# Performance work log

Hardware: AMD Instinct MI355X
Metric: run time of the kernel (lower is better)

## Reference

```python
import jax, jax.numpy as jnp
import numpy as np

N = 50000      # nodes
E = 800000     # edges (before self-loops)
IN_F = 64
HID = 96
OUT_F = 16
L = 16         # num GCN2Conv layers
ALPHA = 0.1
THETA = 0.5


def setup_inputs() -> dict:
    key = jax.random.key(0)
    ks = jax.random.split(key, 6)
    x = jax.random.normal(ks[0], (N, IN_F), jnp.float32)
    edge_index = jax.random.randint(ks[1], (2, E), 0, N, jnp.int64)
    lin0_w = jax.random.normal(ks[2], (HID, IN_F), jnp.float32) * 0.05
    lin0_b = jnp.zeros((HID,), jnp.float32)
    lin1_w = jax.random.normal(ks[3], (OUT_F, HID), jnp.float32) * 0.05
    lin1_b = jnp.zeros((OUT_F,), jnp.float32)
    conv_w = jax.random.normal(ks[4], (L, HID, HID), jnp.float32) * 0.05
    return {"x": x, "edge_index": edge_index, "lin0_w": lin0_w, "lin0_b": lin0_b,
            "lin1_w": lin1_w, "lin1_b": lin1_b, "conv_w": conv_w}


def _gcn_norm(edge_index, n):
    # add self-loops, symmetric normalization D^-1/2 A D^-1/2 (edge weights = 1)
    loops = jnp.arange(n, dtype=edge_index.dtype)
    row = jnp.concatenate([edge_index[0], loops])
    col = jnp.concatenate([edge_index[1], loops])
    ones = jnp.ones(row.shape[0], jnp.float32)
    deg = jax.ops.segment_sum(ones, col, num_segments=n)
    dis = jnp.where(deg > 0, jax.lax.rsqrt(deg), 0.0)
    val = dis[row] * dis[col]
    return row, col, val


def reference(x, edge_index, lin0_w, lin0_b, lin1_w, lin1_b, conv_w):
    n = x.shape[0]
    row, col, val = _gcn_norm(edge_index, n)
    h = jax.nn.relu(x @ lin0_w.T + lin0_b)            # [N, HID]
    x0 = h
    betas = jnp.log(THETA / jnp.arange(1.0, L + 1.0) + 1.0).astype(jnp.float32)

    def layer(h, wb):
        w, beta = wb
        # SpMM: out[i] = sum_{(i,j) in E} val * h[j]
        m = jax.ops.segment_sum(val[:, None] * h[col], row, num_segments=n)
        s = (1.0 - ALPHA) * m + ALPHA * x0            # initial-residual combine
        out = (1.0 - beta) * s + beta * (s @ w)       # identity mapping (shared weights)
        return jax.nn.relu(out), None

    h, _ = jax.lax.scan(layer, h, (conv_w, betas))
    return h @ lin1_w.T + lin1_b
```

## Files before the change

kernel.cpp:

```cpp
#include <hip/hip_runtime.h>

#define NTHREADS 256
#define HID 96
#define INF 64
#define OUTF 16
#define NLAYERS 16
#define NHW 25088
#define CB 128

typedef __attribute__((ext_vector_type(8))) unsigned short ushort8_t;
typedef __attribute__((ext_vector_type(8))) short short8_t;
typedef __attribute__((ext_vector_type(4))) float f32x4_t;

static __device__ __forceinline__ float bf2f(unsigned short u) {
  return __uint_as_float(((unsigned)u) << 16);
}
static __device__ __forceinline__ unsigned short f2bf(float x) {
  unsigned u = __float_as_uint(x);
  return (unsigned short)((u + 0x7FFF + ((u >> 16) & 1)) >> 16);
}
static __device__ __forceinline__ unsigned pack2bf(float a, float b) {
  return (unsigned)f2bf(a) | ((unsigned)f2bf(b) << 16);
}

__global__ __launch_bounds__(NTHREADS) void k_hist(
    const int* __restrict__ idx, int e, unsigned* __restrict__ part, int nw) {
  __shared__ unsigned hh[NHW];
  int tid = threadIdx.x;
  for (int i = tid; i < NHW; i += NTHREADS) hh[i] = 0;
  __syncthreads();
  int per = (e + CB - 1) / CB;
  int s = blockIdx.x * per;
  int en = min(e, s + per);
  for (int i = s + tid; i < en; i += NTHREADS) {
    int v = idx[i];
    atomicAdd(&hh[v >> 1], (v & 1) ? 0x10000u : 1u);
  }
  __syncthreads();
  unsigned* dst = part + (size_t)blockIdx.x * NHW;
  for (int i = tid; i < nw; i += NTHREADS) dst[i] = hh[i];
}

__global__ void k_hmerge(unsigned* __restrict__ partR,
                         const unsigned* __restrict__ partC,
                         int* __restrict__ cnt, int* __restrict__ deg,
                         int n, int nw) {
  int w = blockIdx.x * NTHREADS + threadIdx.x;
  if (w >= nw) return;
  unsigned rl = 0, rh = 0, cl = 0, ch = 0;
#pragma unroll 4
  for (int b = 0; b < CB; ++b) {
    size_t o = (size_t)b * NHW + w;
    unsigned pr = partR[o];
    partR[o] = rl | (rh << 16);
    rl += pr & 0xFFFFu; rh += pr >> 16;
    unsigned pc = partC[o];
    cl += pc & 0xFFFFu; ch += pc >> 16;
  }
  int i0 = 2 * w, i1 = 2 * w + 1;
  if (i0 < n) { cnt[i0] = 1 + (int)rl; deg[i0] = 1 + (int)cl; }
  if (i1 < n) { cnt[i1] = 1 + (int)rh; deg[i1] = 1 + (int)ch; }
}

__global__ void k_dis(const int* __restrict__ deg, float* __restrict__ dis,
                      float* __restrict__ selfval, int n) {
  int i = blockIdx.x * NTHREADS + threadIdx.x;
  if (i < n) {
    float d = (float)deg[i];
    dis[i] = rsqrtf(d);
    selfval[i] = 1.0f / d;
  }
}

__global__ void k_scan1(const int* __restrict__ cnt, int* __restrict__ rp,
                        int* __restrict__ bsum, int n) {
  __shared__ int sh[NTHREADS];
  int t = threadIdx.x;
  int i = blockIdx.x * NTHREADS + t;
  int v = (i < n) ? cnt[i] : 0;
  sh[t] = v;
  __syncthreads();
  for (int ofs = 1; ofs < NTHREADS; ofs <<= 1) {
    int u = (t >= ofs) ? sh[t - ofs] : 0;
    __syncthreads();
    sh[t] += u;
    __syncthreads();
  }
  if (i < n) rp[i] = sh[t] - v;
  if (t == NTHREADS - 1) bsum[blockIdx.x] = sh[t];
}

__global__ void k_scan2(int* __restrict__ bsum, int nb) {
  __shared__ int sh[NTHREADS];
  int t = threadIdx.x;
  int v = (t < nb) ? bsum[t] : 0;
  sh[t] = v;
  __syncthreads();
  for (int ofs = 1; ofs < NTHREADS; ofs <<= 1) {
    int u = (t >= ofs) ? sh[t - ofs] : 0;
    __syncthreads();
    sh[t] += u;
    __syncthreads();
  }
  if (t < nb) bsum[t] = sh[t] - v;
}

__global__ void k_scan3(int* __restrict__ rp, const int* __restrict__ bsum,
                        int n, int etot) {
  int i = blockIdx.x * NTHREADS + threadIdx.x;
  if (i < n) rp[i] += bsum[blockIdx.x];
  if (i == 0) rp[n] = etot;
}

__global__ void k_self(const int* __restrict__ rp, const float* __restrict__ sv,
                       int2* __restrict__ ev, int n) {
  int i = blockIdx.x * NTHREADS + threadIdx.x;
  if (i < n) {
    int2 v;
    v.x = i;
    v.y = __float_as_int(sv[i]);
    ev[rp[i]] = v;
  }
}

__global__ __launch_bounds__(NTHREADS) void k_scatter2(
    const int* __restrict__ row, const int* __restrict__ col,
    const int* __restrict__ rp, const unsigned* __restrict__ prefR,
    const float* __restrict__ dis, int2* __restrict__ ev, int e) {
  __shared__ unsigned lcur[NHW];
  int tid = threadIdx.x;
  for (int i = tid; i < NHW; i += NTHREADS) lcur[i] = 0;
  __syncthreads();
  int per = (e + CB - 1) / CB;
  int s = blockIdx.x * per;
  int en = min(e, s + per);
  const unsigned* pref = prefR + (size_t)blockIdx.x * NHW;
  for (int i = s + tid; i < en; i += NTHREADS) {
    int r = row[i], c = col[i];
    unsigned old = atomicAdd(&lcur[r >> 1], (r & 1) ? 0x10000u : 1u);
    unsigned loc = (r & 1) ? (old >> 16) : (old & 0xFFFFu);
    unsigned pw = pref[r >> 1];
    unsigned pb = (r & 1) ? (pw >> 16) : (pw & 0xFFFFu);
    int p = rp[r] + 1 + (int)pb + (int)loc;
    int2 v;
    v.x = c;
    v.y = __float_as_int(dis[r] * dis[c]);
    ev[p] = v;
  }
}

__global__ void k_wprime(const float* __restrict__ cw,
                         unsigned short* __restrict__ wTb) {
  int l = blockIdx.y;
  int idx = blockIdx.x * NTHREADS + threadIdx.x;
  int f = idx / HID, k = idx % HID;
  wTb[l * HID * HID + idx] = f2bf(cw[l * HID * HID + k * HID + f]);
}

__global__ __launch_bounds__(NTHREADS) void k_lin0(
    const float* __restrict__ x, const float* __restrict__ w0,
    const float* __restrict__ b0, unsigned short* __restrict__ x0b, int n) {
  __shared__ float wl[INF * HID];
  __shared__ float xT[INF * 68];
  int tid = threadIdx.x;
#pragma unroll
  for (int i = 0; i < 6; ++i) {
    int idx = tid + i * NTHREADS;
    int hrow = idx / 16, q = idx % 16;
    float4 v = *(const float4*)(w0 + hrow * INF + q * 4);
    wl[(q * 4 + 0) * HID + hrow] = v.x;
    wl[(q * 4 + 1) * HID + hrow] = v.y;
    wl[(q * 4 + 2) * HID + hrow] = v.z;
    wl[(q * 4 + 3) * HID + hrow] = v.w;
  }
  int r0 = blockIdx.x * 64;
#pragma unroll
  for (int i = 0; i < 4; ++i) {
    int idx = tid + i * NTHREADS;
    int r = idx / 16, q = idx % 16;
    int gr = r0 + r;
    float4 v = make_float4(0.f, 0.f, 0.f, 0.f);
    if (gr < n) v = *(const float4*)(x + (size_t)gr * INF + q * 4);
    xT[(q * 4 + 0) * 68 + r] = v.x;
    xT[(q * 4 + 1) * 68 + r] = v.y;
    xT[(q * 4 + 2) * 68 + r] = v.z;
    xT[(q * 4 + 3) * 68 + r] = v.w;
  }
  __syncthreads();
  int rg = tid & 15, cg = tid >> 4;
  float acc[4][6];
#pragma unroll
  for (int i = 0; i < 4; ++i)
#pragma unroll
    for (int j = 0; j < 6; ++j) acc[i][j] = 0.f;
#pragma unroll 4
  for (int k = 0; k < INF; ++k) {
    float4 s4 = *(const float4*)(xT + k * 68 + rg * 4);
    const float2* w2 = (const float2*)(wl + k * HID + cg * 6);
    float2 wa = w2[0], wb = w2[1], wc = w2[2];
    float wv[6] = {wa.x, wa.y, wb.x, wb.y, wc.x, wc.y};
    float sv[4] = {s4.x, s4.y, s4.z, s4.w};
#pragma unroll
    for (int i = 0; i < 4; ++i)
#pragma unroll
      for (int j = 0; j < 6; ++j) acc[i][j] = fmaf(sv[i], wv[j], acc[i][j]);
  }
  float bb[6];
#pragma unroll
  for (int j = 0; j < 6; ++j) bb[j] = b0[cg * 6 + j];
#pragma unroll
  for (int i = 0; i < 4; ++i) {
    int gr = r0 + rg * 4 + i;
    if (gr < n) {
      float r_[6];
#pragma unroll
      for (int j = 0; j < 6; ++j) r_[j] = fmaxf(acc[i][j] + bb[j], 0.f);
      unsigned* ob = (unsigned*)(x0b + (size_t)gr * HID + cg * 6);
      ob[0] = pack2bf(r_[0], r_[1]);
      ob[1] = pack2bf(r_[2], r_[3]);
      ob[2] = pack2bf(r_[4], r_[5]);
    }
  }
}

__global__ __launch_bounds__(NTHREADS) void k_layer(
    const unsigned short* __restrict__ hin, const unsigned short* __restrict__ x0,
    const int* __restrict__ rp, const int2* __restrict__ ev,
    const unsigned short* __restrict__ wT, unsigned short* __restrict__ hout,
    float omb, float beta, int n) {
  __shared__ unsigned char pool[38912] __attribute__((aligned(16)));
  float* red = (float*)pool;
  unsigned short* wl = (unsigned short*)pool;
  unsigned short* sT = (unsigned short*)(pool + 25600);
  int tid = threadIdx.x;
  int hw = tid >> 5, lane = tid & 31;
  int eb = lane >> 2, fg = lane & 3;
  int r0 = blockIdx.x * 64;

  for (int sub = 0; sub < 8; ++sub) {
    int rl = sub * 8 + hw;
    int r = r0 + rl;
    if (r >= n) r = n - 1;
    int e0 = rp[r], e1 = rp[r + 1];
    float acc[24];
#pragma unroll
    for (int j = 0; j < 24; ++j) acc[j] = 0.f;
    int idx0 = e0 + eb;
    bool ok = idx0 < e1;
    idx0 = ok ? idx0 : e1 - 1;
    int2 cv = ev[idx0];
    for (int base = e0; base < e1; base += 8) {
      int2 cur = cv;
      bool okc = ok;
      int nb = base + 8;
      if (nb < e1) {
        int i2 = nb + eb;
        ok = i2 < e1;
        i2 = ok ? i2 : e1 - 1;
        cv = ev[i2];
      }
      float v = okc ? __int_as_float(cur.y) : 0.f;
      const unsigned short* hc = hin + (size_t)cur.x * HID + fg * 24;
      ushort8_t p0 = *(const ushort8_t*)(hc);
      ushort8_t p1 = *(const ushort8_t*)(hc + 8);
      ushort8_t p2 = *(const ushort8_t*)(hc + 16);
#pragma unroll
      for (int j = 0; j < 8; ++j) acc[j]      = fmaf(v, bf2f(p0[j]), acc[j]);
#pragma unroll
      for (int j = 0; j < 8; ++j) acc[8 + j]  = fmaf(v, bf2f(p1[j]), acc[8 + j]);
#pragma unroll
      for (int j = 0; j < 8; ++j) acc[16 + j] = fmaf(v, bf2f(p2[j]), acc[16 + j]);
    }
    float* myr = red + (hw * 8 + eb) * 100 + fg * 24;
#pragma unroll
    for (int j = 0; j < 6; ++j)
      *(float4*)(myr + j * 4) =
          make_float4(acc[j * 4], acc[j * 4 + 1], acc[j * 4 + 2], acc[j * 4 + 3]);
    asm volatile("s_waitcnt lgkmcnt(0)" ::: "memory");
    __builtin_amdgcn_wave_barrier();
    if (lane < 24) {
      const float* base = red + hw * 800 + lane * 4;
      float4 tot = *(const float4*)(base);
#pragma unroll
      for (int b = 1; b < 8; ++b) {
        float4 p = *(const float4*)(base + b * 100);
        tot.x += p.x; tot.y += p.y; tot.z += p.z; tot.w += p.w;
      }
      const unsigned* xr = (const unsigned*)(x0 + (size_t)r * HID + lane * 4);
      unsigned xa = xr[0], xb = xr[1];
      float s0 = 0.9f * tot.x + 0.1f * bf2f((unsigned short)(xa & 0xFFFFu));
      float s1 = 0.9f * tot.y + 0.1f * bf2f((unsigned short)(xa >> 16));
      float s2 = 0.9f * tot.z + 0.1f * bf2f((unsigned short)(xb & 0xFFFFu));
      float s3 = 0.9f * tot.w + 0.1f * bf2f((unsigned short)(xb >> 16));
      unsigned* op = (unsigned*)(sT + rl * 104 + lane * 4);
      op[0] = pack2bf(s0, s1);
      op[1] = pack2bf(s2, s3);
    }
    asm volatile("" ::: "memory");
    __builtin_amdgcn_wave_barrier();
  }
  __syncthreads();
#pragma unroll
  for (int i = 0; i < 5; ++i) {
    int idx = tid + i * NTHREADS;
    if (idx < 1152) {
      int f = idx / 12, c = (idx % 12) * 8;
      *(ushort8_t*)(wl + f * 104 + c) = *(const ushort8_t*)(wT + f * HID + c);
    }
  }
  __syncthreads();
  int lane64 = tid & 63, wave = tid >> 6;
  int l15 = lane64 & 15;
  int kg = lane64 >> 4;
  f32x4_t acc2[6];
#pragma unroll
  for (int i = 0; i < 6; ++i) acc2[i] = (f32x4_t)(0.f);
#pragma unroll
  for (int kt = 0; kt < 3; ++kt) {
    short8_t A = *(const short8_t*)(sT + (wave * 16 + l15) * 104 + kt * 32 + kg * 8);
#pragma unroll
    for (int ft = 0; ft < 6; ++ft) {
      short8_t B = *(const short8_t*)(wl + (ft * 16 + l15) * 104 + kt * 32 + kg * 8);
      acc2[ft] = __builtin_amdgcn_mfma_f32_16x16x32_bf16(A, B, acc2[ft], 0, 0, 0);
    }
  }
#pragma unroll
  for (int ft = 0; ft < 6; ++ft) {
    int col = ft * 16 + l15;
#pragma unroll
    for (int j = 0; j < 4; ++j) {
      int rl = wave * 16 + kg * 4 + j;
      int gr = r0 + rl;
      float sv = bf2f(sT[rl * 104 + col]);
      float o = fmaxf(omb * sv + beta * acc2[ft][j], 0.f);
      if (gr < n) hout[(size_t)gr * HID + col] = f2bf(o);
    }
  }
}

__global__ __launch_bounds__(NTHREADS) void k_lin1(
    const unsigned short* __restrict__ h, const float* __restrict__ w1,
    const float* __restrict__ b1, float* __restrict__ out, int n) {
  __shared__ float hT[HID * 68];
  __shared__ float w1l[HID * OUTF];
  int tid = threadIdx.x;
#pragma unroll
  for (int i = 0; i < 6; ++i) {
    int idx = tid + i * NTHREADS;
    int o = idx / HID, k = idx % HID;
    w1l[k * OUTF + o] = w1[idx];
  }
  int r0 = blockIdx.x * 64;
#pragma unroll
  for (int i = 0; i < 3; ++i) {
    int idx = tid + i * NTHREADS;
    int r = idx / 12, q = idx % 12;
    int gr = r0 + r;
    ushort8_t v = (ushort8_t)0;
    if (gr < n) v = *(const ushort8_t*)(h + (size_t)gr * HID + q * 8);
#pragma unroll
    for (int j = 0; j < 8; ++j) hT[(q * 8 + j) * 68 + r] = bf2f(v[j]);
  }
  __syncthreads();
  int r = tid & 63, og = tid >> 6;
  float acc[4] = {0.f, 0.f, 0.f, 0.f};
#pragma unroll 4
  for (int k = 0; k < HID; ++k) {
    float s = hT[k * 68 + r];
    float4 w4 = *(const float4*)(w1l + k * OUTF + og * 4);
    acc[0] = fmaf(s, w4.x, acc[0]);
    acc[1] = fmaf(s, w4.y, acc[1]);
    acc[2] = fmaf(s, w4.z, acc[2]);
    acc[3] = fmaf(s, w4.w, acc[3]);
  }
  int gr = r0 + r;
  if (gr < n) {
    float* op = out + (size_t)gr * OUTF + og * 4;
#pragma unroll
    for (int j = 0; j < 4; ++j) op[j] = acc[j] + b1[og * 4 + j];
  }
}

extern "C" void kernel_launch(void* const* d_in, const int* in_sizes, int n_in,
                              void* d_out, int out_size, void* d_ws, size_t ws_size,
                              hipStream_t stream) {
  const float* x  = (const float*)d_in[0];
  const int*   ei = (const int*)d_in[1];
  const float* w0 = (const float*)d_in[2];
  const float* b0 = (const float*)d_in[3];
  const float* w1 = (const float*)d_in[4];
  const float* b1 = (const float*)d_in[5];
  const float* cw = (const float*)d_in[6];
  int n = in_sizes[0] / INF;
  int e = in_sizes[1] / 2;
  const int* row = ei;
  const int* col = ei + e;

  char* ws = (char*)d_ws;
  size_t off = 0;
  auto alloc = [&](size_t bytes) -> void* {
    void* p = (void*)(ws + off);
    off += (bytes + 255) & ~(size_t)255;
    return p;
  };
  unsigned short* x0b = (unsigned short*)alloc((size_t)n * HID * 2);
  unsigned short* hbA = (unsigned short*)alloc((size_t)n * HID * 2);
  unsigned short* hbB = (unsigned short*)alloc((size_t)n * HID * 2);
  unsigned short* wTb = (unsigned short*)alloc((size_t)NLAYERS * HID * HID * 2);
  int*   deg  = (int*)alloc((size_t)n * 4);
  float* dis  = (float*)alloc((size_t)n * 4);
  float* sv   = (float*)alloc((size_t)n * 4);
  int*   cnt  = (int*)alloc((size_t)n * 4);
  int*   rp   = (int*)alloc((size_t)(n + 1) * 4);
  int2*  ev   = (int2*)alloc((size_t)(e + n) * 8);
  int*   bsum = (int*)alloc(1024 * 4);
  unsigned* partR = (unsigned*)x0b;
  unsigned* partC = partR + (size_t)CB * NHW;
  int nw = (n + 1) / 2;
  (void)ws_size; (void)n_in; (void)out_size;

  int nb  = (n + NTHREADS - 1) / NTHREADS;
  int r64 = (n + 63) / 64;

  k_hist<<<CB, NTHREADS, 0, stream>>>(row, e, partR, nw);
  k_hist<<<CB, NTHREADS, 0, stream>>>(col, e, partC, nw);
  k_hmerge<<<(nw + NTHREADS - 1) / NTHREADS, NTHREADS, 0, stream>>>(
      partR, partC, cnt, deg, n, nw);
  k_dis<<<nb, NTHREADS, 0, stream>>>(deg, dis, sv, n);
  k_scan1<<<nb, NTHREADS, 0, stream>>>(cnt, rp, bsum, n);
  k_scan2<<<1, NTHREADS, 0, stream>>>(bsum, nb);
  k_scan3<<<nb, NTHREADS, 0, stream>>>(rp, bsum, n, e + n);
  k_self<<<nb, NTHREADS, 0, stream>>>(rp, sv, ev, n);
  k_scatter2<<<CB, NTHREADS, 0, stream>>>(row, col, rp, partR, dis, ev, e);
  k_wprime<<<dim3(36, NLAYERS), NTHREADS, 0, stream>>>(cw, wTb);
  k_lin0<<<r64, NTHREADS, 0, stream>>>(x, w0, b0, x0b, n);

  const unsigned short* hin = x0b;
  for (int l = 0; l < NLAYERS; ++l) {
    unsigned short* hout = (l & 1) ? hbB : hbA;
    float beta = logf(0.5f / (float)(l + 1) + 1.0f);
    k_layer<<<r64, NTHREADS, 0, stream>>>(hin, x0b, rp, ev,
                                          wTb + (size_t)l * HID * HID, hout,
                                          1.0f - beta, beta, n);
    hin = hout;
  }
  k_lin1<<<r64, NTHREADS, 0, stream>>>(hin, w1, b1, (float*)d_out, n);
}
```

Measured before the change: 646.6 us.

## Factor symmetric normalization into pre-scaled features and drop per-edge weights

Rewrites D^-1/2 A D^-1/2 aggregation so each layer stores features already scaled by dis, and the destination scale is applied once per row. The edge list then holds only column indices (4 bytes instead of 8), which halves edge-array traffic in every layer. The dis kernel is merged into hmerge and the self-loop fill into scan3, removing two launches. lin1 rescales by sqrt(deg) to undo the scaling. This adds extra bf16 rounding from storing scaled features, which may change accuracy slightly.

```diff
diff --git a/kernel.cpp b/kernel.cpp
--- a/kernel.cpp
+++ b/kernel.cpp
@@ -43,8 +43,8 @@
 
 __global__ void k_hmerge(unsigned* __restrict__ partR,
                          const unsigned* __restrict__ partC,
-                         int* __restrict__ cnt, int* __restrict__ deg,
-                         int n, int nw) {
+                         int* __restrict__ cnt, float* __restrict__ dis,
+                         float* __restrict__ rdis, int n, int nw) {
   int w = blockIdx.x * NTHREADS + threadIdx.x;
   if (w >= nw) return;
   unsigned rl = 0, rh = 0, cl = 0, ch = 0;
@@ -58,17 +58,15 @@
     cl += pc & 0xFFFFu; ch += pc >> 16;
   }
   int i0 = 2 * w, i1 = 2 * w + 1;
-  if (i0 < n) { cnt[i0] = 1 + (int)rl; deg[i0] = 1 + (int)cl; }
-  if (i1 < n) { cnt[i1] = 1 + (int)rh; deg[i1] = 1 + (int)ch; }
-}
-
-__global__ void k_dis(const int* __restrict__ deg, float* __restrict__ dis,
-                      float* __restrict__ selfval, int n) {
-  int i = blockIdx.x * NTHREADS + threadIdx.x;
-  if (i < n) {
-    float d = (float)deg[i];
-    dis[i] = rsqrtf(d);
-    selfval[i] = 1.0f / d;
+  if (i0 < n) {
+    cnt[i0] = 1 + (int)rl;
+    float d = (float)(1 + (int)cl);
+    dis[i0] = rsqrtf(d); rdis[i0] = sqrtf(d);
+  }
+  if (i1 < n) {
+    cnt[i1] = 1 + (int)rh;
+    float d = (float)(1 + (int)ch);
+    dis[i1] = rsqrtf(d); rdis[i1] = sqrtf(d);
   }
 }
 
@@ -106,27 +104,20 @@
 }
 
 __global__ void k_scan3(int* __restrict__ rp, const int* __restrict__ bsum,
-                        int n, int etot) {
-  int i = blockIdx.x * NTHREADS + threadIdx.x;
-  if (i < n) rp[i] += bsum[blockIdx.x];
-  if (i == 0) rp[n] = etot;
-}
-
-__global__ void k_self(const int* __restrict__ rp, const float* __restrict__ sv,
-                       int2* __restrict__ ev, int n) {
+                        int* __restrict__ ev, int n, int etot) {
   int i = blockIdx.x * NTHREADS + threadIdx.x;
   if (i < n) {
-    int2 v;
-    v.x = i;
-    v.y = __float_as_int(sv[i]);
-    ev[rp[i]] = v;
-  }
-}
-
-__global__ __launch_bounds__(NTHREADS) void k_scatter2(
+    int v = rp[i] + bsum[blockIdx.x];
+    rp[i] = v;
+    ev[v] = i;
+  }
+  if (i == 0) rp[n] = etot;
+}
+
+__global__ __launch_bounds__(NTHREADS) void k_scatter3(
     const int* __restrict__ row, const int* __restrict__ col,
     const int* __restrict__ rp, const unsigned* __restrict__ prefR,
-    const float* __restrict__ dis, int2* __restrict__ ev, int e) {
+    int* __restrict__ ev, int e) {
   __shared__ unsigned lcur[NHW];
   int tid = threadIdx.x;
   for (int i = tid; i < NHW; i += NTHREADS) lcur[i] = 0;
@@ -141,11 +132,7 @@
     unsigned loc = (r & 1) ? (old >> 16) : (old & 0xFFFFu);
     unsigned pw = pref[r >> 1];
     unsigned pb = (r & 1) ? (pw >> 16) : (pw & 0xFFFFu);
-    int p = rp[r] + 1 + (int)pb + (int)loc;
-    int2 v;
-    v.x = c;
-    v.y = __float_as_int(dis[r] * dis[c]);
-    ev[p] = v;
+    ev[rp[r] + 1 + (int)pb + (int)loc] = c;
   }
 }
 
@@ -159,7 +146,8 @@
 
 __global__ __launch_bounds__(NTHREADS) void k_lin0(
     const float* __restrict__ x, const float* __restrict__ w0,
-    const float* __restrict__ b0, unsigned short* __restrict__ x0b, int n) {
+    const float* __restrict__ b0, const float* __restrict__ dis,
+    unsigned short* __restrict__ x0b, unsigned short* __restrict__ hs0, int n) {
   __shared__ float wl[INF * HID];
   __shared__ float xT[INF * 68];
   int tid = threadIdx.x;
@@ -215,19 +203,24 @@
       float r_[6];
 #pragma unroll
       for (int j = 0; j < 6; ++j) r_[j] = fmaxf(acc[i][j] + bb[j], 0.f);
+      float dr = dis[gr];
       unsigned* ob = (unsigned*)(x0b + (size_t)gr * HID + cg * 6);
       ob[0] = pack2bf(r_[0], r_[1]);
       ob[1] = pack2bf(r_[2], r_[3]);
       ob[2] = pack2bf(r_[4], r_[5]);
+      unsigned* oh = (unsigned*)(hs0 + (size_t)gr * HID + cg * 6);
+      oh[0] = pack2bf(dr * r_[0], dr * r_[1]);
+      oh[1] = pack2bf(dr * r_[2], dr * r_[3]);
+      oh[2] = pack2bf(dr * r_[4], dr * r_[5]);
     }
   }
 }
 
 __global__ __launch_bounds__(NTHREADS) void k_layer(
-    const unsigned short* __restrict__ hin, const unsigned short* __restrict__ x0,
-    const int* __restrict__ rp, const int2* __restrict__ ev,
-    const unsigned short* __restrict__ wT, unsigned short* __restrict__ hout,
-    float omb, float beta, int n) {
+    const unsigned short* __restrict__ hs, const unsigned short* __restrict__ x0,
+    const float* __restrict__ dis, const int* __restrict__ rp,
+    const int* __restrict__ ev, const unsigned short* __restrict__ wT,
+    unsigned short* __restrict__ hsout, float omb, float beta, int n) {
   __shared__ unsigned char pool[38912] __attribute__((aligned(16)));
   float* red = (float*)pool;
   unsigned short* wl = (unsigned short*)pool;
@@ -248,9 +241,9 @@
     int idx0 = e0 + eb;
     bool ok = idx0 < e1;
     idx0 = ok ? idx0 : e1 - 1;
-    int2 cv = ev[idx0];
+    int cv = ev[idx0];
     for (int base = e0; base < e1; base += 8) {
-      int2 cur = cv;
+      int cur = cv;
       bool okc = ok;
       int nb = base + 8;
       if (nb < e1) {
@@ -259,8 +252,8 @@
         i2 = ok ? i2 : e1 - 1;
         cv = ev[i2];
       }
-      float v = okc ? __int_as_float(cur.y) : 0.f;
-      const unsigned short* hc = hin + (size_t)cur.x * HID + fg * 24;
+      float v = okc ? 1.f : 0.f;
+      const unsigned short* hc = hs + (size_t)cur * HID + fg * 24;
       ushort8_t p0 = *(const ushort8_t*)(hc);
       ushort8_t p1 = *(const ushort8_t*)(hc + 8);
       ushort8_t p2 = *(const ushort8_t*)(hc + 16);
@@ -286,12 +279,13 @@
         float4 p = *(const float4*)(base + b * 100);
         tot.x += p.x; tot.y += p.y; tot.z += p.z; tot.w += p.w;
       }
+      float w09 = 0.9f * dis[r];
       const unsigned* xr = (const unsigned*)(x0 + (size_t)r * HID + lane * 4);
       unsigned xa = xr[0], xb = xr[1];
-      float s0 = 0.9f * tot.x + 0.1f * bf2f((unsigned short)(xa & 0xFFFFu));
-      float s1 = 0.9f * tot.y + 0.1f * bf2f((unsigned short)(xa >> 16));
-      float s2 = 0.9f * tot.z + 0.1f * bf2f((unsigned short)(xb & 0xFFFFu));
-      float s3 = 0.9f * tot.w + 0.1f * bf2f((unsigned short)(xb >> 16));
+      float s0 = w09 * tot.x + 0.1f * bf2f((unsigned short)(xa & 0xFFFFu));
+      float s1 = w09 * tot.y + 0.1f * bf2f((unsigned short)(xa >> 16));
+      float s2 = w09 * tot.z + 0.1f * bf2f((unsigned short)(xb & 0xFFFFu));
+      float s3 = w09 * tot.w + 0.1f * bf2f((unsigned short)(xb >> 16));
       unsigned* op = (unsigned*)(sT + rl * 104 + lane * 4);
       op[0] = pack2bf(s0, s1);
       op[1] = pack2bf(s2, s3);
@@ -331,16 +325,19 @@
     for (int j = 0; j < 4; ++j) {
       int rl = wave * 16 + kg * 4 + j;
       int gr = r0 + rl;
-      float sv = bf2f(sT[rl * 104 + col]);
-      float o = fmaxf(omb * sv + beta * acc2[ft][j], 0.f);
-      if (gr < n) hout[(size_t)gr * HID + col] = f2bf(o);
+      if (gr < n) {
+        float sv = bf2f(sT[rl * 104 + col]);
+        float o = fmaxf(omb * sv + beta * acc2[ft][j], 0.f);
+        hsout[(size_t)gr * HID + col] = f2bf(dis[gr] * o);
+      }
     }
   }
 }
 
 __global__ __launch_bounds__(NTHREADS) void k_lin1(
-    const unsigned short* __restrict__ h, const float* __restrict__ w1,
-    const float* __restrict__ b1, float* __restrict__ out, int n) {
+    const unsigned short* __restrict__ hs, const float* __restrict__ rdis,
+    const float* __restrict__ w1, const float* __restrict__ b1,
+    float* __restrict__ out, int n) {
   __shared__ float hT[HID * 68];
   __shared__ float w1l[HID * OUTF];
   int tid = threadIdx.x;
@@ -357,9 +354,13 @@
     int r = idx / 12, q = idx % 12;
     int gr = r0 + r;
     ushort8_t v = (ushort8_t)0;
-    if (gr < n) v = *(const ushort8_t*)(h + (size_t)gr * HID + q * 8);
-#pragma unroll
-    for (int j = 0; j < 8; ++j) hT[(q * 8 + j) * 68 + r] = bf2f(v[j]);
+    float sc = 0.f;
+    if (gr < n) {
+      v = *(const ushort8_t*)(hs + (size_t)gr * HID + q * 8);
+      sc = rdis[gr];
+    }
+#pragma unroll
+    for (int j = 0; j < 8; ++j) hT[(q * 8 + j) * 68 + r] = sc * bf2f(v[j]);
   }
   __syncthreads();
   int r = tid & 63, og = tid >> 6;
@@ -404,15 +405,14 @@
     return p;
   };
   unsigned short* x0b = (unsigned short*)alloc((size_t)n * HID * 2);
-  unsigned short* hbA = (unsigned short*)alloc((size_t)n * HID * 2);
-  unsigned short* hbB = (unsigned short*)alloc((size_t)n * HID * 2);
+  unsigned short* hsA = (unsigned short*)alloc((size_t)n * HID * 2);
+  unsigned short* hsB = (unsigned short*)alloc((size_t)n * HID * 2);
   unsigned short* wTb = (unsigned short*)alloc((size_t)NLAYERS * HID * HID * 2);
-  int*   deg  = (int*)alloc((size_t)n * 4);
   float* dis  = (float*)alloc((size_t)n * 4);
-  float* sv   = (float*)alloc((size_t)n * 4);
+  float* rdis = (float*)alloc((size_t)n * 4);
   int*   cnt  = (int*)alloc((size_t)n * 4);
   int*   rp   = (int*)alloc((size_t)(n + 1) * 4);
-  int2*  ev   = (int2*)alloc((size_t)(e + n) * 8);
+  int*   ev   = (int*)alloc((size_t)(e + n) * 4);
   int*   bsum = (int*)alloc(1024 * 4);
   unsigned* partR = (unsigned*)x0b;
   unsigned* partC = partR + (size_t)CB * NHW;
@@ -425,24 +425,22 @@
   k_hist<<<CB, NTHREADS, 0, stream>>>(row, e, partR, nw);
   k_hist<<<CB, NTHREADS, 0, stream>>>(col, e, partC, nw);
   k_hmerge<<<(nw + NTHREADS - 1) / NTHREADS, NTHREADS, 0, stream>>>(
-      partR, partC, cnt, deg, n, nw);
-  k_dis<<<nb, NTHREADS, 0, stream>>>(deg, dis, sv, n);
+      partR, partC, cnt, dis, rdis, n, nw);
   k_scan1<<<nb, NTHREADS, 0, stream>>>(cnt, rp, bsum, n);
   k_scan2<<<1, NTHREADS, 0, stream>>>(bsum, nb);
-  k_scan3<<<nb, NTHREADS, 0, stream>>>(rp, bsum, n, e + n);
-  k_self<<<nb, NTHREADS, 0, stream>>>(rp, sv, ev, n);
-  k_scatter2<<<CB, NTHREADS, 0, stream>>>(row, col, rp, partR, dis, ev, e);
+  k_scan3<<<nb, NTHREADS, 0, stream>>>(rp, bsum, ev, n, e + n);
+  k_scatter3<<<CB, NTHREADS, 0, stream>>>(row, col, rp, partR, ev, e);
   k_wprime<<<dim3(36, NLAYERS), NTHREADS, 0, stream>>>(cw, wTb);
-  k_lin0<<<r64, NTHREADS, 0, stream>>>(x, w0, b0, x0b, n);
-
-  const unsigned short* hin = x0b;
+  k_lin0<<<r64, NTHREADS, 0, stream>>>(x, w0, b0, dis, x0b, hsA, n);
+
+  const unsigned short* hin = hsA;
   for (int l = 0; l < NLAYERS; ++l) {
-    unsigned short* hout = (l & 1) ? hbB : hbA;
+    unsigned short* hout = (l & 1) ? hsA : hsB;
     float beta = logf(0.5f / (float)(l + 1) + 1.0f);
-    k_layer<<<r64, NTHREADS, 0, stream>>>(hin, x0b, rp, ev,
+    k_layer<<<r64, NTHREADS, 0, stream>>>(hin, x0b, dis, rp, ev,
                                           wTb + (size_t)l * HID * HID, hout,
                                           1.0f - beta, beta, n);
     hin = hout;
   }
-  k_lin1<<<r64, NTHREADS, 0, stream>>>(hin, w1, b1, (float*)d_out, n);
-}
+  k_lin1<<<r64, NTHREADS, 0, stream>>>(hin, rdis, w1, b1, (float*)d_out, n);
+}
```

Result: slower. 660.9 us (+2.2%).
